# Optimization experiments

Hardware: AMD Instinct MI355X
Metric: run time of the kernel (lower is better)

Reference implementation:

```python
import jax, jax.numpy as jnp
import numpy as np


def setup_inputs() -> dict:
    N, E, F_IN, H, C = 100000, 3200000, 128, 16, 2
    key = jax.random.key(0)
    k1, k2, k3, k4 = jax.random.split(key, 4)
    x = jax.random.normal(k1, (N, F_IN), dtype=jnp.float32)
    edge_index = jax.random.randint(k2, (2, E), 0, N, dtype=jnp.int64)
    W1 = jax.random.normal(k3, (F_IN, H), dtype=jnp.float32) * (1.0 / np.sqrt(F_IN))
    b1 = jnp.zeros((H,), dtype=jnp.float32)
    W2 = jax.random.normal(k4, (H, C), dtype=jnp.float32) * (1.0 / np.sqrt(H))
    b2 = jnp.zeros((C,), dtype=jnp.float32)
    return {"x": x, "edge_index": edge_index, "W1": W1, "b1": b1, "W2": W2, "b2": b2}


def _gcn_norm(edge_index, num_nodes):
    # PyG gcn_norm: add self-loops, deg from destination, norm = d^-1/2[src]*d^-1/2[dst]
    loop = jnp.arange(num_nodes, dtype=edge_index.dtype)
    src = jnp.concatenate([edge_index[0], loop])
    dst = jnp.concatenate([edge_index[1], loop])
    deg = jax.ops.segment_sum(jnp.ones_like(src, dtype=jnp.float32), dst,
                              num_segments=num_nodes)
    dinv = jnp.where(deg > 0, jax.lax.rsqrt(deg), 0.0)
    norm = dinv[src] * dinv[dst]  # [E + N]
    return src, dst, norm


def _gcn_conv(h, src, dst, norm, W, b, num_nodes):
    h = h @ W                       # dense transform first (in >= out channels)
    msg = h[src] * norm[:, None]    # gather + normalize, [E+N, out]
    agg = jax.ops.segment_sum(msg, dst, num_segments=num_nodes)
    return agg + b


def reference(x, edge_index, W1, b1, W2, b2):
    N = x.shape[0]
    src, dst, norm = _gcn_norm(edge_index, N)
    h = jax.nn.relu(_gcn_conv(x, src, dst, norm, W1, b1, N))
    out = _gcn_conv(h, src, dst, norm, W2, b2, N)
    return out
```

## Files before the change

kernel.cpp:

```cpp
#include <hip/hip_runtime.h>


#define EPB  8192
#define RCAP 12288
#define CAP  16384

typedef unsigned int u32;
typedef unsigned short u16;

__device__ __forceinline__ float bflo(u32 u) { return __uint_as_float(u << 16); }
__device__ __forceinline__ float bfhi(u32 u) { return __uint_as_float(u & 0xffff0000u); }
__device__ __forceinline__ u32 pack_bf2(float a, float b) {
    u32 ua = __float_as_uint(a); ua = (ua + 0x7fffu + ((ua >> 16) & 1u)) >> 16;
    u32 ub = __float_as_uint(b); ub = (ub + 0x7fffu + ((ub >> 16) & 1u)) >> 16;
    return ua | (ub << 16);
}

__global__ __launch_bounds__(512) void k_binit(int* __restrict__ gcur, int NBUK) {
    int t = threadIdx.x;
    if (t < NBUK) gcur[t] = t * RCAP;
}

__global__ __launch_bounds__(512) void k_scatter(const int* __restrict__ ei,
                                                 int* __restrict__ gcur,
                                                 u32* __restrict__ part,
                                                 int E, int NBUK) {
    __shared__ int hist[512];
    __shared__ int rbase[512];
    __shared__ u32 buf[EPB];
    __shared__ u16 bkt[EPB];
    int tid = threadIdx.x;
    hist[tid] = 0;
    __syncthreads();
    int base = blockIdx.x * EPB;
    int end = base + EPB; if (end > E) end = E;
    int cnt = end - base;
    int nv = cnt >> 2;
    const int4* s4p = (const int4*)(ei + base);
    const int4* d4p = (const int4*)(ei + E + base);
    int4 s4[4], d4[4];
    #pragma unroll
    for (int k = 0; k < 4; ++k) {
        int idx = tid + (k << 9);
        if (idx < nv) {
            s4[k] = s4p[idx];
            d4[k] = d4p[idx];
            atomicAdd(&hist[d4[k].x >> 8], 1);
            atomicAdd(&hist[d4[k].y >> 8], 1);
            atomicAdd(&hist[d4[k].z >> 8], 1);
            atomicAdd(&hist[d4[k].w >> 8], 1);
        }
    }
    for (int e = base + (nv << 2) + tid; e < end; e += 512)
        atomicAdd(&hist[ei[E + e] >> 8], 1);
    __syncthreads();
    int v = hist[tid];
    __syncthreads();
    for (int o = 1; o < 512; o <<= 1) {
        int t = (tid >= o) ? hist[tid - o] : 0;
        __syncthreads();
        hist[tid] += t;
        __syncthreads();
    }
    int excl = hist[tid] - v;
    int rb = 0;
    if (tid < NBUK && v > 0) rb = atomicAdd(&gcur[tid], v);
    rbase[tid] = rb - excl;
    __syncthreads();
    hist[tid] = excl;
    __syncthreads();
    #pragma unroll
    for (int k = 0; k < 4; ++k) {
        int idx = tid + (k << 9);
        if (idx < nv) {
            int b, pos;
            b = d4[k].x >> 8; pos = atomicAdd(&hist[b], 1);
            buf[pos] = ((u32)(d4[k].x & 255) << 24) | (u32)s4[k].x; bkt[pos] = (u16)b;
            b = d4[k].y >> 8; pos = atomicAdd(&hist[b], 1);
            buf[pos] = ((u32)(d4[k].y & 255) << 24) | (u32)s4[k].y; bkt[pos] = (u16)b;
            b = d4[k].z >> 8; pos = atomicAdd(&hist[b], 1);
            buf[pos] = ((u32)(d4[k].z & 255) << 24) | (u32)s4[k].z; bkt[pos] = (u16)b;
            b = d4[k].w >> 8; pos = atomicAdd(&hist[b], 1);
            buf[pos] = ((u32)(d4[k].w & 255) << 24) | (u32)s4[k].w; bkt[pos] = (u16)b;
        }
    }
    for (int e = base + (nv << 2) + tid; e < end; e += 512) {
        int s = ei[e], d = ei[E + e];
        int b = d >> 8;
        int pos = atomicAdd(&hist[b], 1);
        buf[pos] = ((u32)(d & 255) << 24) | (u32)s;
        bkt[pos] = (u16)b;
    }
    __syncthreads();
    for (int j = tid; j < cnt; j += 512)
        part[rbase[bkt[j]] + j] = buf[j];
}

__global__ __launch_bounds__(512) void k_fillB(const u32* __restrict__ part,
                                               const int* __restrict__ gcur,
                                               u32* __restrict__ csr,
                                               int* __restrict__ rp,
                                               float* __restrict__ dinv,
                                               int N, int E, int NBUK) {
    __shared__ int hist[256];
    __shared__ int ofs[256];
    __shared__ int bs[512];
    __shared__ u32 srcbuf[CAP];
    int b = blockIdx.x, tid = threadIdx.x;
    if (b == 0 && tid == 0) rp[N] = E;
    int vb = (tid < NBUK) ? (gcur[tid] - tid * RCAP) : 0;
    bs[tid] = vb;
    if (tid < 256) hist[tid] = 0;
    __syncthreads();
    for (int o = 1; o < 512; o <<= 1) {
        int t = (tid >= o) ? bs[tid - o] : 0;
        __syncthreads();
        bs[tid] += t;
        __syncthreads();
    }
    int cnt = gcur[b] - b * RCAP;
    int base_w = bs[b] - cnt;
    int base_r = b * RCAP;
    int nv = cnt >> 2;
    const uint4* p4 = (const uint4*)(part + base_r);
    for (int t = tid; t < nv; t += 512) {
        uint4 pv = p4[t];
        atomicAdd(&hist[pv.x >> 24], 1);
        atomicAdd(&hist[pv.y >> 24], 1);
        atomicAdd(&hist[pv.z >> 24], 1);
        atomicAdd(&hist[pv.w >> 24], 1);
    }
    for (int j = (nv << 2) + tid; j < cnt; j += 512)
        atomicAdd(&hist[part[base_r + j] >> 24], 1);
    __syncthreads();
    int v = 0;
    if (tid < 256) { v = hist[tid]; ofs[tid] = v; }
    __syncthreads();
    for (int o = 1; o < 256; o <<= 1) {
        int t = 0;
        if (tid < 256 && tid >= o) t = ofs[tid - o];
        __syncthreads();
        if (tid < 256) ofs[tid] += t;
        __syncthreads();
    }
    int excl = 0;
    if (tid < 256) { excl = ofs[tid] - v; hist[tid] = excl; }
    __syncthreads();
    for (int t = tid; t < nv; t += 512) {
        uint4 pv = p4[t];
        int pos;
        pos = atomicAdd(&hist[pv.x >> 24], 1);
        if (pos < CAP) srcbuf[pos] = pv.x & 0xFFFFFFu;
        pos = atomicAdd(&hist[pv.y >> 24], 1);
        if (pos < CAP) srcbuf[pos] = pv.y & 0xFFFFFFu;
        pos = atomicAdd(&hist[pv.z >> 24], 1);
        if (pos < CAP) srcbuf[pos] = pv.z & 0xFFFFFFu;
        pos = atomicAdd(&hist[pv.w >> 24], 1);
        if (pos < CAP) srcbuf[pos] = pv.w & 0xFFFFFFu;
    }
    for (int j = (nv << 2) + tid; j < cnt; j += 512) {
        u32 pv = part[base_r + j];
        int pos = atomicAdd(&hist[pv >> 24], 1);
        if (pos < CAP) srcbuf[pos] = pv & 0xFFFFFFu;
    }
    __syncthreads();
    for (int j = tid; j < cnt; j += 512)
        csr[base_w + j] = srcbuf[j];
    int d = b * 256 + tid;
    if (tid < 256 && d < N) {
        rp[d] = base_w + excl;
        dinv[d] = rsqrtf((float)(v + 1));
    }
}

__global__ __launch_bounds__(256) void k_xw1(const float* __restrict__ x,
                                             const float* __restrict__ W1,
                                             const float* __restrict__ dinv,
                                             u16* __restrict__ hs, int N) {
    __shared__ float w[4 * 516];
    int tid = threadIdx.x;
    for (int t = tid; t < 2048; t += 256)
        w[(t >> 9) * 516 + (t & 511)] = W1[t];
    __syncthreads();
    int t = blockIdx.x * 256 + tid;
    int n = t >> 2, q = t & 3;
    if (n >= N) return;
    const float4* xr = (const float4*)(x + (size_t)n * 128 + q * 32);
    const float* ws = w + q * 516;
    float acc[16];
    #pragma unroll
    for (int c = 0; c < 16; ++c) acc[c] = 0.f;
    #pragma unroll
    for (int i = 0; i < 8; ++i) {
        float4 u = xr[i];
        const float4* wf = (const float4*)(ws + i * 64);
        #pragma unroll
        for (int c4 = 0; c4 < 4; ++c4) {
            float4 wa = wf[c4];
            float4 wb = wf[4 + c4];
            float4 wc = wf[8 + c4];
            float4 wd = wf[12 + c4];
            int c = c4 * 4;
            acc[c+0] = fmaf(u.x, wa.x, acc[c+0]); acc[c+1] = fmaf(u.x, wa.y, acc[c+1]);
            acc[c+2] = fmaf(u.x, wa.z, acc[c+2]); acc[c+3] = fmaf(u.x, wa.w, acc[c+3]);
            acc[c+0] = fmaf(u.y, wb.x, acc[c+0]); acc[c+1] = fmaf(u.y, wb.y, acc[c+1]);
            acc[c+2] = fmaf(u.y, wb.z, acc[c+2]); acc[c+3] = fmaf(u.y, wb.w, acc[c+3]);
            acc[c+0] = fmaf(u.z, wc.x, acc[c+0]); acc[c+1] = fmaf(u.z, wc.y, acc[c+1]);
            acc[c+2] = fmaf(u.z, wc.z, acc[c+2]); acc[c+3] = fmaf(u.z, wc.w, acc[c+3]);
            acc[c+0] = fmaf(u.w, wd.x, acc[c+0]); acc[c+1] = fmaf(u.w, wd.y, acc[c+1]);
            acc[c+2] = fmaf(u.w, wd.z, acc[c+2]); acc[c+3] = fmaf(u.w, wd.w, acc[c+3]);
        }
    }
    #pragma unroll
    for (int c = 0; c < 16; ++c) {
        acc[c] += __shfl_xor(acc[c], 1);
        acc[c] += __shfl_xor(acc[c], 2);
    }
    float di = dinv[n];
    uint2 o;
    o.x = pack_bf2(acc[4*q+0] * di, acc[4*q+1] * di);
    o.y = pack_bf2(acc[4*q+2] * di, acc[4*q+3] * di);
    ((uint2*)(hs + (size_t)n * 16))[q] = o;
}

__global__ __launch_bounds__(256) void k_agg1h2(const int* __restrict__ rp,
                                                const int* __restrict__ csr,
                                                const u16* __restrict__ hs,
                                                const float* __restrict__ dinv,
                                                const float* __restrict__ W2,
                                                const float* __restrict__ b1,
                                                float* __restrict__ h2s, int N) {
    int lane = threadIdx.x & 63;
    int wid = blockIdx.x * 16 + (threadIdx.x >> 6) * 4 + (lane >> 4);
    if (wid >= N) return;
    int l = lane & 15;
    int half = l & 1, g = l >> 1;
    int beg = rp[wid], end = rp[wid + 1];
    float a0 = 0.f, a1 = 0.f, a2 = 0.f, a3 = 0.f;
    float a4 = 0.f, a5 = 0.f, a6 = 0.f, a7 = 0.f;
    for (int j = beg + g; j < end; j += 8) {
        int s = csr[j];
        uint4 u = ((const uint4*)(hs + (size_t)s * 16))[half];
        a0 += bflo(u.x); a1 += bfhi(u.x);
        a2 += bflo(u.y); a3 += bfhi(u.y);
        a4 += bflo(u.z); a5 += bfhi(u.z);
        a6 += bflo(u.w); a7 += bfhi(u.w);
    }
    a0 += __shfl_xor(a0, 2); a1 += __shfl_xor(a1, 2);
    a2 += __shfl_xor(a2, 2); a3 += __shfl_xor(a3, 2);
    a4 += __shfl_xor(a4, 2); a5 += __shfl_xor(a5, 2);
    a6 += __shfl_xor(a6, 2); a7 += __shfl_xor(a7, 2);
    a0 += __shfl_xor(a0, 4); a1 += __shfl_xor(a1, 4);
    a2 += __shfl_xor(a2, 4); a3 += __shfl_xor(a3, 4);
    a4 += __shfl_xor(a4, 4); a5 += __shfl_xor(a5, 4);
    a6 += __shfl_xor(a6, 4); a7 += __shfl_xor(a7, 4);
    a0 += __shfl_xor(a0, 8); a1 += __shfl_xor(a1, 8);
    a2 += __shfl_xor(a2, 8); a3 += __shfl_xor(a3, 8);
    a4 += __shfl_xor(a4, 8); a5 += __shfl_xor(a5, 8);
    a6 += __shfl_xor(a6, 8); a7 += __shfl_xor(a7, 8);
    uint4 su = ((const uint4*)(hs + (size_t)wid * 16))[half];
    a0 += bflo(su.x); a1 += bfhi(su.x);
    a2 += bflo(su.y); a3 += bfhi(su.y);
    a4 += bflo(su.z); a5 += bfhi(su.z);
    a6 += bflo(su.w); a7 += bfhi(su.w);
    float di = dinv[wid];
    float4 bA = ((const float4*)b1)[half * 2];
    float4 bB = ((const float4*)b1)[half * 2 + 1];
    float v0 = fmaxf(fmaf(di, a0, bA.x), 0.f);
    float v1 = fmaxf(fmaf(di, a1, bA.y), 0.f);
    float v2 = fmaxf(fmaf(di, a2, bA.z), 0.f);
    float v3 = fmaxf(fmaf(di, a3, bA.w), 0.f);
    float v4 = fmaxf(fmaf(di, a4, bB.x), 0.f);
    float v5 = fmaxf(fmaf(di, a5, bB.y), 0.f);
    float v6 = fmaxf(fmaf(di, a6, bB.z), 0.f);
    float v7 = fmaxf(fmaf(di, a7, bB.w), 0.f);
    const float4* w4 = (const float4*)W2 + half * 4;
    float4 q0 = w4[0], q1 = w4[1], q2 = w4[2], q3 = w4[3];
    float p0 = v0*q0.x + v1*q0.z + v2*q1.x + v3*q1.z
             + v4*q2.x + v5*q2.z + v6*q3.x + v7*q3.z;
    float p1 = v0*q0.y + v1*q0.w + v2*q1.y + v3*q1.w
             + v4*q2.y + v5*q2.w + v6*q3.y + v7*q3.w;
    p0 += __shfl_xor(p0, 1); p1 += __shfl_xor(p1, 1);
    if (l == 0)
        *(float2*)(h2s + (size_t)wid * 2) = make_float2(p0 * di, p1 * di);
}

__global__ __launch_bounds__(256) void k_agg2(const int* __restrict__ rp,
                                              const int* __restrict__ csr,
                                              const float* __restrict__ h2s,
                                              const float* __restrict__ dinv,
                                              const float* __restrict__ b2,
                                              float* __restrict__ out, int N) {
    int lane = threadIdx.x & 63;
    int wid = blockIdx.x * 16 + (threadIdx.x >> 6) * 4 + (lane >> 4);
    if (wid >= N) return;
    int l = lane & 15;
    int beg = rp[wid], end = rp[wid + 1];
    float a0 = 0.f, a1 = 0.f;
    for (int j = beg + l; j < end; j += 16) {
        int s = csr[j];
        float2 v = *(const float2*)(h2s + (size_t)s * 2);
        a0 += v.x; a1 += v.y;
    }
    a0 += __shfl_xor(a0, 1); a1 += __shfl_xor(a1, 1);
    a0 += __shfl_xor(a0, 2); a1 += __shfl_xor(a1, 2);
    a0 += __shfl_xor(a0, 4); a1 += __shfl_xor(a1, 4);
    a0 += __shfl_xor(a0, 8); a1 += __shfl_xor(a1, 8);
    if (l == 0) {
        float di = dinv[wid];
        float2 sv = *(const float2*)(h2s + (size_t)wid * 2);
        *(float2*)(out + (size_t)wid * 2) =
            make_float2(fmaf(di, a0 + sv.x, b2[0]), fmaf(di, a1 + sv.y, b2[1]));
    }
}

extern "C" void kernel_launch(void* const* d_in, const int* in_sizes, int n_in,
                              void* d_out, int out_size, void* d_ws, size_t ws_size,
                              hipStream_t stream) {
    const float* x  = (const float*)d_in[0];
    const int*   ei = (const int*)d_in[1];
    const float* W1 = (const float*)d_in[2];
    const float* b1 = (const float*)d_in[3];
    const float* W2 = (const float*)d_in[4];
    const float* b2 = (const float*)d_in[5];
    float* out = (float*)d_out;

    const int N = in_sizes[0] / 128;
    const int E = in_sizes[1] / 2;
    const int NBUK = (N + 255) / 256;
    const int NPB  = (E + EPB - 1) / EPB;

    char* ws = (char*)d_ws;
    size_t off = 0;
    auto alloc = [&](size_t bytes) {
        void* p = ws + off;
        off = (off + bytes + 255) & ~(size_t)255;
        return p;
    };
    u32*   part  = (u32*)alloc((size_t)NBUK * RCAP * 4);
    u32*   csr   = (u32*)alloc((size_t)E * 4);
    int*   rp    = (int*)alloc((size_t)(N + 1) * 4);
    float* dinv  = (float*)alloc((size_t)N * 4);
    u16*   hs    = (u16*)alloc((size_t)N * 16 * 2);
    float* h2s   = (float*)alloc((size_t)N * 2 * 4);
    int*   gcur  = (int*)alloc((size_t)NBUK * 4);

    k_binit  <<<dim3(1),    dim3(512), 0, stream>>>(gcur, NBUK);
    k_scatter<<<dim3(NPB),  dim3(512), 0, stream>>>(ei, gcur, part, E, NBUK);
    k_fillB  <<<dim3(NBUK), dim3(512), 0, stream>>>(part, gcur, csr, rp, dinv, N, E, NBUK);
    k_xw1    <<<dim3((N * 4 + 255) / 256), dim3(256), 0, stream>>>(x, W1, dinv, hs, N);
    k_agg1h2 <<<dim3((N + 15) / 16), dim3(256), 0, stream>>>(rp, (const int*)csr, hs, dinv, W2, b1, h2s, N);
    k_agg2   <<<dim3((N + 15) / 16), dim3(256), 0, stream>>>(rp, (const int*)csr, h2s, dinv, b2, out, N);
}
```

Baseline: 188.3 us.

## Run X·W1 concurrently with edge scatter in one fused launch, scale in fillB

```diff
diff --git a/kernel.cpp b/kernel.cpp
--- a/kernel.cpp
+++ b/kernel.cpp
@@ -21,79 +21,124 @@
     if (t < NBUK) gcur[t] = t * RCAP;
 }
 
-__global__ __launch_bounds__(512) void k_scatter(const int* __restrict__ ei,
-                                                 int* __restrict__ gcur,
-                                                 u32* __restrict__ part,
-                                                 int E, int NBUK) {
-    __shared__ int hist[512];
-    __shared__ int rbase[512];
-    __shared__ u32 buf[EPB];
-    __shared__ u16 bkt[EPB];
+__global__ __launch_bounds__(512) void k_fat(const int* __restrict__ ei,
+                                             int* __restrict__ gcur,
+                                             u32* __restrict__ part,
+                                             const float* __restrict__ x,
+                                             const float* __restrict__ W1,
+                                             float* __restrict__ hraw,
+                                             int E, int NBUK, int NSCAT, int N) {
+    __shared__ union {
+        struct { int hist[512]; int rbase[512]; u32 buf[EPB]; u16 bkt[EPB]; } s;
+        float w[4 * 516];
+    } sm;
     int tid = threadIdx.x;
-    hist[tid] = 0;
-    __syncthreads();
-    int base = blockIdx.x * EPB;
-    int end = base + EPB; if (end > E) end = E;
-    int cnt = end - base;
-    int nv = cnt >> 2;
-    const int4* s4p = (const int4*)(ei + base);
-    const int4* d4p = (const int4*)(ei + E + base);
-    int4 s4[4], d4[4];
-    #pragma unroll
-    for (int k = 0; k < 4; ++k) {
-        int idx = tid + (k << 9);
-        if (idx < nv) {
-            s4[k] = s4p[idx];
-            d4[k] = d4p[idx];
-            atomicAdd(&hist[d4[k].x >> 8], 1);
-            atomicAdd(&hist[d4[k].y >> 8], 1);
-            atomicAdd(&hist[d4[k].z >> 8], 1);
-            atomicAdd(&hist[d4[k].w >> 8], 1);
-        }
-    }
-    for (int e = base + (nv << 2) + tid; e < end; e += 512)
-        atomicAdd(&hist[ei[E + e] >> 8], 1);
-    __syncthreads();
-    int v = hist[tid];
-    __syncthreads();
-    for (int o = 1; o < 512; o <<= 1) {
-        int t = (tid >= o) ? hist[tid - o] : 0;
-        __syncthreads();
-        hist[tid] += t;
-        __syncthreads();
-    }
-    int excl = hist[tid] - v;
-    int rb = 0;
-    if (tid < NBUK && v > 0) rb = atomicAdd(&gcur[tid], v);
-    rbase[tid] = rb - excl;
-    __syncthreads();
-    hist[tid] = excl;
-    __syncthreads();
-    #pragma unroll
-    for (int k = 0; k < 4; ++k) {
-        int idx = tid + (k << 9);
-        if (idx < nv) {
-            int b, pos;
-            b = d4[k].x >> 8; pos = atomicAdd(&hist[b], 1);
-            buf[pos] = ((u32)(d4[k].x & 255) << 24) | (u32)s4[k].x; bkt[pos] = (u16)b;
-            b = d4[k].y >> 8; pos = atomicAdd(&hist[b], 1);
-            buf[pos] = ((u32)(d4[k].y & 255) << 24) | (u32)s4[k].y; bkt[pos] = (u16)b;
-            b = d4[k].z >> 8; pos = atomicAdd(&hist[b], 1);
-            buf[pos] = ((u32)(d4[k].z & 255) << 24) | (u32)s4[k].z; bkt[pos] = (u16)b;
-            b = d4[k].w >> 8; pos = atomicAdd(&hist[b], 1);
-            buf[pos] = ((u32)(d4[k].w & 255) << 24) | (u32)s4[k].w; bkt[pos] = (u16)b;
-        }
-    }
-    for (int e = base + (nv << 2) + tid; e < end; e += 512) {
-        int s = ei[e], d = ei[E + e];
-        int b = d >> 8;
-        int pos = atomicAdd(&hist[b], 1);
-        buf[pos] = ((u32)(d & 255) << 24) | (u32)s;
-        bkt[pos] = (u16)b;
-    }
-    __syncthreads();
-    for (int j = tid; j < cnt; j += 512)
-        part[rbase[bkt[j]] + j] = buf[j];
+    if ((int)blockIdx.x < NSCAT) {
+        sm.s.hist[tid] = 0;
+        __syncthreads();
+        int base = blockIdx.x * EPB;
+        int end = base + EPB; if (end > E) end = E;
+        int cnt = end - base;
+        int nv = cnt >> 2;
+        const int4* s4p = (const int4*)(ei + base);
+        const int4* d4p = (const int4*)(ei + E + base);
+        int4 s4[4], d4[4];
+        #pragma unroll
+        for (int k = 0; k < 4; ++k) {
+            int idx = tid + (k << 9);
+            if (idx < nv) {
+                s4[k] = s4p[idx];
+                d4[k] = d4p[idx];
+                atomicAdd(&sm.s.hist[d4[k].x >> 8], 1);
+                atomicAdd(&sm.s.hist[d4[k].y >> 8], 1);
+                atomicAdd(&sm.s.hist[d4[k].z >> 8], 1);
+                atomicAdd(&sm.s.hist[d4[k].w >> 8], 1);
+            }
+        }
+        for (int e = base + (nv << 2) + tid; e < end; e += 512)
+            atomicAdd(&sm.s.hist[ei[E + e] >> 8], 1);
+        __syncthreads();
+        int v = sm.s.hist[tid];
+        __syncthreads();
+        for (int o = 1; o < 512; o <<= 1) {
+            int t = (tid >= o) ? sm.s.hist[tid - o] : 0;
+            __syncthreads();
+            sm.s.hist[tid] += t;
+            __syncthreads();
+        }
+        int excl = sm.s.hist[tid] - v;
+        int rb = 0;
+        if (tid < NBUK && v > 0) rb = atomicAdd(&gcur[tid], v);
+        sm.s.rbase[tid] = rb - excl;
+        __syncthreads();
+        sm.s.hist[tid] = excl;
+        __syncthreads();
+        #pragma unroll
+        for (int k = 0; k < 4; ++k) {
+            int idx = tid + (k << 9);
+            if (idx < nv) {
+                int b, pos;
+                b = d4[k].x >> 8; pos = atomicAdd(&sm.s.hist[b], 1);
+                sm.s.buf[pos] = ((u32)(d4[k].x & 255) << 24) | (u32)s4[k].x; sm.s.bkt[pos] = (u16)b;
+                b = d4[k].y >> 8; pos = atomicAdd(&sm.s.hist[b], 1);
+                sm.s.buf[pos] = ((u32)(d4[k].y & 255) << 24) | (u32)s4[k].y; sm.s.bkt[pos] = (u16)b;
+                b = d4[k].z >> 8; pos = atomicAdd(&sm.s.hist[b], 1);
+                sm.s.buf[pos] = ((u32)(d4[k].z & 255) << 24) | (u32)s4[k].z; sm.s.bkt[pos] = (u16)b;
+                b = d4[k].w >> 8; pos = atomicAdd(&sm.s.hist[b], 1);
+                sm.s.buf[pos] = ((u32)(d4[k].w & 255) << 24) | (u32)s4[k].w; sm.s.bkt[pos] = (u16)b;
+            }
+        }
+        for (int e = base + (nv << 2) + tid; e < end; e += 512) {
+            int s = ei[e], d = ei[E + e];
+            int b = d >> 8;
+            int pos = atomicAdd(&sm.s.hist[b], 1);
+            sm.s.buf[pos] = ((u32)(d & 255) << 24) | (u32)s;
+            sm.s.bkt[pos] = (u16)b;
+        }
+        __syncthreads();
+        for (int j = tid; j < cnt; j += 512)
+            part[sm.s.rbase[sm.s.bkt[j]] + j] = sm.s.buf[j];
+    } else {
+        for (int t = tid; t < 2048; t += 512)
+            sm.w[(t >> 9) * 516 + (t & 511)] = W1[t];
+        __syncthreads();
+        int t = ((int)blockIdx.x - NSCAT) * 512 + tid;
+        int n = t >> 2, q = t & 3;
+        if (n >= N) return;
+        const float4* xr = (const float4*)(x + (size_t)n * 128 + q * 32);
+        const float* ws = sm.w + q * 516;
+        float acc[16];
+        #pragma unroll
+        for (int c = 0; c < 16; ++c) acc[c] = 0.f;
+        #pragma unroll
+        for (int i = 0; i < 8; ++i) {
+            float4 u = xr[i];
+            const float4* wf = (const float4*)(ws + i * 64);
+            #pragma unroll
+            for (int c4 = 0; c4 < 4; ++c4) {
+                float4 wa = wf[c4];
+                float4 wb = wf[4 + c4];
+                float4 wc = wf[8 + c4];
+                float4 wd = wf[12 + c4];
+                int c = c4 * 4;
+                acc[c+0] = fmaf(u.x, wa.x, acc[c+0]); acc[c+1] = fmaf(u.x, wa.y, acc[c+1]);
+                acc[c+2] = fmaf(u.x, wa.z, acc[c+2]); acc[c+3] = fmaf(u.x, wa.w, acc[c+3]);
+                acc[c+0] = fmaf(u.y, wb.x, acc[c+0]); acc[c+1] = fmaf(u.y, wb.y, acc[c+1]);
+                acc[c+2] = fmaf(u.y, wb.z, acc[c+2]); acc[c+3] = fmaf(u.y, wb.w, acc[c+3]);
+                acc[c+0] = fmaf(u.z, wc.x, acc[c+0]); acc[c+1] = fmaf(u.z, wc.y, acc[c+1]);
+                acc[c+2] = fmaf(u.z, wc.z, acc[c+2]); acc[c+3] = fmaf(u.z, wc.w, acc[c+3]);
+                acc[c+0] = fmaf(u.w, wd.x, acc[c+0]); acc[c+1] = fmaf(u.w, wd.y, acc[c+1]);
+                acc[c+2] = fmaf(u.w, wd.z, acc[c+2]); acc[c+3] = fmaf(u.w, wd.w, acc[c+3]);
+            }
+        }
+        #pragma unroll
+        for (int c = 0; c < 16; ++c) {
+            acc[c] += __shfl_xor(acc[c], 1);
+            acc[c] += __shfl_xor(acc[c], 2);
+        }
+        ((float4*)(hraw + (size_t)n * 16))[q] =
+            make_float4(acc[4*q+0], acc[4*q+1], acc[4*q+2], acc[4*q+3]);
+    }
 }
 
 __global__ __launch_bounds__(512) void k_fillB(const u32* __restrict__ part,
@@ -101,6 +146,8 @@
                                                u32* __restrict__ csr,
                                                int* __restrict__ rp,
                                                float* __restrict__ dinv,
+                                               const float* __restrict__ hraw,
+                                               u16* __restrict__ hs,
                                                int N, int E, int NBUK) {
     __shared__ int hist[256];
     __shared__ int ofs[256];
@@ -169,58 +216,24 @@
     int d = b * 256 + tid;
     if (tid < 256 && d < N) {
         rp[d] = base_w + excl;
-        dinv[d] = rsqrtf((float)(v + 1));
-    }
-}
-
-__global__ __launch_bounds__(256) void k_xw1(const float* __restrict__ x,
-                                             const float* __restrict__ W1,
-                                             const float* __restrict__ dinv,
-                                             u16* __restrict__ hs, int N) {
-    __shared__ float w[4 * 516];
-    int tid = threadIdx.x;
-    for (int t = tid; t < 2048; t += 256)
-        w[(t >> 9) * 516 + (t & 511)] = W1[t];
-    __syncthreads();
-    int t = blockIdx.x * 256 + tid;
-    int n = t >> 2, q = t & 3;
-    if (n >= N) return;
-    const float4* xr = (const float4*)(x + (size_t)n * 128 + q * 32);
-    const float* ws = w + q * 516;
-    float acc[16];
-    #pragma unroll
-    for (int c = 0; c < 16; ++c) acc[c] = 0.f;
-    #pragma unroll
-    for (int i = 0; i < 8; ++i) {
-        float4 u = xr[i];
-        const float4* wf = (const float4*)(ws + i * 64);
-        #pragma unroll
-        for (int c4 = 0; c4 < 4; ++c4) {
-            float4 wa = wf[c4];
-            float4 wb = wf[4 + c4];
-            float4 wc = wf[8 + c4];
-            float4 wd = wf[12 + c4];
-            int c = c4 * 4;
-            acc[c+0] = fmaf(u.x, wa.x, acc[c+0]); acc[c+1] = fmaf(u.x, wa.y, acc[c+1]);
-            acc[c+2] = fmaf(u.x, wa.z, acc[c+2]); acc[c+3] = fmaf(u.x, wa.w, acc[c+3]);
-            acc[c+0] = fmaf(u.y, wb.x, acc[c+0]); acc[c+1] = fmaf(u.y, wb.y, acc[c+1]);
-            acc[c+2] = fmaf(u.y, wb.z, acc[c+2]); acc[c+3] = fmaf(u.y, wb.w, acc[c+3]);
-            acc[c+0] = fmaf(u.z, wc.x, acc[c+0]); acc[c+1] = fmaf(u.z, wc.y, acc[c+1]);
-            acc[c+2] = fmaf(u.z, wc.z, acc[c+2]); acc[c+3] = fmaf(u.z, wc.w, acc[c+3]);
-            acc[c+0] = fmaf(u.w, wd.x, acc[c+0]); acc[c+1] = fmaf(u.w, wd.y, acc[c+1]);
-            acc[c+2] = fmaf(u.w, wd.z, acc[c+2]); acc[c+3] = fmaf(u.w, wd.w, acc[c+3]);
-        }
-    }
-    #pragma unroll
-    for (int c = 0; c < 16; ++c) {
-        acc[c] += __shfl_xor(acc[c], 1);
-        acc[c] += __shfl_xor(acc[c], 2);
-    }
-    float di = dinv[n];
-    uint2 o;
-    o.x = pack_bf2(acc[4*q+0] * di, acc[4*q+1] * di);
-    o.y = pack_bf2(acc[4*q+2] * di, acc[4*q+3] * di);
-    ((uint2*)(hs + (size_t)n * 16))[q] = o;
+        float dval = rsqrtf((float)(v + 1));
+        dinv[d] = dval;
+        ((float*)ofs)[tid] = dval;
+    }
+    __syncthreads();
+    int dn = b * 256 + (tid >> 1);
+    if (dn < N) {
+        float di = ((float*)ofs)[tid >> 1];
+        int h = tid & 1;
+        const float4* hr = (const float4*)(hraw + (size_t)dn * 16);
+        float4 A = hr[h * 2], B = hr[h * 2 + 1];
+        uint4 o;
+        o.x = pack_bf2(A.x * di, A.y * di);
+        o.y = pack_bf2(A.z * di, A.w * di);
+        o.z = pack_bf2(B.x * di, B.y * di);
+        o.w = pack_bf2(B.z * di, B.w * di);
+        ((uint4*)(hs + (size_t)dn * 16))[h] = o;
+    }
 }
 
 __global__ __launch_bounds__(256) void k_agg1h2(const int* __restrict__ rp,
@@ -329,6 +342,7 @@
     const int E = in_sizes[1] / 2;
     const int NBUK = (N + 255) / 256;
     const int NPB  = (E + EPB - 1) / EPB;
+    const int NXW  = (N * 4 + 511) / 512;
 
     char* ws = (char*)d_ws;
     size_t off = 0;
@@ -341,14 +355,14 @@
     u32*   csr   = (u32*)alloc((size_t)E * 4);
     int*   rp    = (int*)alloc((size_t)(N + 1) * 4);
     float* dinv  = (float*)alloc((size_t)N * 4);
+    float* hraw  = (float*)alloc((size_t)N * 16 * 4);
     u16*   hs    = (u16*)alloc((size_t)N * 16 * 2);
     float* h2s   = (float*)alloc((size_t)N * 2 * 4);
     int*   gcur  = (int*)alloc((size_t)NBUK * 4);
 
-    k_binit  <<<dim3(1),    dim3(512), 0, stream>>>(gcur, NBUK);
-    k_scatter<<<dim3(NPB),  dim3(512), 0, stream>>>(ei, gcur, part, E, NBUK);
-    k_fillB  <<<dim3(NBUK), dim3(512), 0, stream>>>(part, gcur, csr, rp, dinv, N, E, NBUK);
-    k_xw1    <<<dim3((N * 4 + 255) / 256), dim3(256), 0, stream>>>(x, W1, dinv, hs, N);
+    k_binit  <<<dim3(1),          dim3(512), 0, stream>>>(gcur, NBUK);
+    k_fat    <<<dim3(NPB + NXW),  dim3(512), 0, stream>>>(ei, gcur, part, x, W1, hraw, E, NBUK, NPB, N);
+    k_fillB  <<<dim3(NBUK),       dim3(512), 0, stream>>>(part, gcur, csr, rp, dinv, hraw, hs, N, E, NBUK);
     k_agg1h2 <<<dim3((N + 15) / 16), dim3(256), 0, stream>>>(rp, (const int*)csr, hs, dinv, W2, b1, h2s, N);
     k_agg2   <<<dim3((N + 15) / 16), dim3(256), 0, stream>>>(rp, (const int*)csr, h2s, dinv, b2, out, N);
 }
```

Measured after the change: 179.2 us. 1.05x faster.
